# Optimization experiments

Measured on AMD Instinct MI355X. Metric: run time of the kernel, lower is better.

The kernel has to match this reference:

```python
import jax, jax.numpy as jnp
import numpy as np

Q_HEADS, KV_HEADS, DIMS = 16, 4, 1024
HEAD_DIM = DIMS // Q_HEADS          # 64
GROUPS = Q_HEADS // KV_HEADS        # 4


def rope(x):
    # x: [..., s, d]; base-10 thetas, positions start at 1 (per source RoPE)
    s, d = x.shape[-2], x.shape[-1]
    thetas = 10.0 ** (-jnp.arange(d // 2, dtype=jnp.float32))
    angles = jnp.arange(1, s + 1, dtype=jnp.float32)[:, None] * thetas  # [s, d/2]
    cos, sin = jnp.cos(angles), jnp.sin(angles)
    xr, xi = x[..., ::2], x[..., 1::2]
    outr = xr * cos - xi * sin
    outi = xr * sin + xi * cos
    return jnp.stack([outr, outi], axis=-1).reshape(x.shape)  # re-interleave


def setup_inputs() -> dict:
    key = jax.random.key(0)
    ks = jax.random.split(key, 5)
    b, s, in_dim = 4, 2048, 1024
    q = jax.random.normal(ks[0], (b, s, in_dim), dtype=jnp.float32)
    mask = jnp.tril(jnp.ones((s, s), dtype=jnp.float32))  # 1 = keep, 0 = masked
    sc = 1.0 / np.sqrt(in_dim)
    Wq = jax.random.normal(ks[1], (in_dim, Q_HEADS, HEAD_DIM), dtype=jnp.float32) * sc
    Wk = jax.random.normal(ks[2], (in_dim, KV_HEADS, HEAD_DIM), dtype=jnp.float32) * sc
    Wv = jax.random.normal(ks[3], (in_dim, KV_HEADS, HEAD_DIM), dtype=jnp.float32) * sc
    Wo = jax.random.normal(ks[4], (KV_HEADS * HEAD_DIM, in_dim), dtype=jnp.float32) * (1.0 / np.sqrt(KV_HEADS * HEAD_DIM))
    return {"q": q, "mask": mask, "Wq": Wq, "Wk": Wk, "Wv": Wv, "Wo": Wo}


def reference(q, mask, Wq, Wk, Wv, Wo):
    b, s, in_dim = q.shape
    # projections (DenseGeneral, no bias)
    qh = jnp.einsum('bsi,ihd->bshd', q, Wq)   # [b, s, 16, 64]
    kh = jnp.einsum('bsi,ihd->bshd', q, Wk)   # [b, s, 4, 64]  (kv = q)
    vh = jnp.einsum('bsi,ihd->bshd', q, Wv)
    # '... s (h g) d -> ... g h s d' with g=GROUPS
    qh = qh.reshape(b, s, KV_HEADS, GROUPS, HEAD_DIM).transpose(0, 3, 2, 1, 4)  # [b,g,h,s,d]
    kh = kh.transpose(0, 2, 1, 3)  # [b, h, s, d]
    vh = vh.transpose(0, 2, 1, 3)
    qh = rope(qh)
    kh = rope(kh)
    # NOTE: source einsum sums over group axis g
    scores = jnp.einsum('bghsd,bhad->bhsa', qh, kh)  # [b, h, s, s]
    scores = scores - (1.0 / mask - 1.0)             # mask==0 -> -inf
    attn = jax.nn.softmax(scores / jnp.float32(HEAD_DIM ** 0.5), axis=-1)
    out = jnp.einsum('bhsa,bhad->bhsd', attn, vh)    # [b, h, s, d]
    out = out.transpose(0, 2, 1, 3).reshape(b, s, KV_HEADS * HEAD_DIM)
    return out @ Wo  # [b, s, in_dim]
```

## Files before the change

### kernel.cpp

```cpp
#include <hip/hip_runtime.h>
#include <math.h>

#define BATCH 4
#define SEQ   2048
#define DIN   1024
#define KVH   4
#define HD    64
#define MTOT  (BATCH*SEQ)
#define NPROJ 768
#define PROJ_STRIDE (BATCH*KVH*SEQ*HD)
#define NCHUNK_TOT 80

typedef unsigned short ushort_t;
typedef __attribute__((ext_vector_type(8))) short short8;
typedef __attribute__((ext_vector_type(4))) float f32x4;

#define QSCALE (0.125f * 1.44269504088896340736f)

__device__ inline ushort_t f2bf(float x) {
    union { float f; unsigned int u; } v; v.f = x;
    unsigned int r = v.u + 0x7fffu + ((v.u >> 16) & 1u);
    return (ushort_t)(r >> 16);
}
__device__ inline ushort_t f2bf_trunc(float x) {
    return (ushort_t)(__float_as_uint(x) >> 16);
}

__device__ inline void load16_lds(const ushort_t* g, ushort_t* l) {
    __builtin_amdgcn_global_load_lds(
        (const __attribute__((address_space(1))) void*)g,
        (__attribute__((address_space(3))) void*)l, 16, 0, 0);
}

__global__ __launch_bounds__(256) void prep_kernel(
        const float* __restrict__ Wq, const float* __restrict__ Wk,
        const float* __restrict__ Wv, const float* __restrict__ Wo,
        const float* __restrict__ X,
        ushort_t* __restrict__ Wcat_t, ushort_t* __restrict__ Wo_t,
        float2* __restrict__ ctab, ushort_t* __restrict__ Y) {
    const int bx = blockIdx.x;
    const int tid = threadIdx.x;
    if (bx < 4096) {
        int idx = bx * 256 + tid;
        if (idx < NPROJ * DIN) {
            int n = idx >> 10, k = idx & 1023;
            float v;
            if (n < 256) {
                const float* p = Wq + (size_t)k * 1024 + (n >> 6) * 256 + (n & 63);
                v = p[0] + p[64] + p[128] + p[192];
            } else if (n < 512) {
                v = Wk[(size_t)k * 256 + (n - 256)];
            } else {
                v = Wv[(size_t)k * 256 + (n - 512)];
            }
            Wcat_t[idx] = f2bf(v);
        } else {
            int t = idx - NPROJ * DIN;
            int n = t >> 8, k = t & 255;
            Wo_t[t] = f2bf(Wo[(size_t)k * 1024 + n]);
        }
    } else if (bx < 4352) {
        int t = (bx - 4096) * 256 + tid;
        int j = t & 31, s = t >> 5;
        float ang = (float)(s + 1) * exp10f(-(float)j);
        float sn, cs;
        sincosf(ang, &sn, &cs);
        ctab[t] = make_float2(cs, sn);
    } else {
        int i = ((bx - 4352) * 256 + tid) * 4;
        float4 v = *(const float4*)&X[i];
        ushort4 o;
        o.x = f2bf(v.x); o.y = f2bf(v.y); o.z = f2bf(v.z); o.w = f2bf(v.w);
        *(ushort4*)&Y[i] = o;
    }
}

template<int OUT_MODE>
__global__ __launch_bounds__(256) void gemm_mfma_kernel(
        const ushort_t* __restrict__ A, const ushort_t* __restrict__ Bt,
        float* __restrict__ Y, ushort_t* __restrict__ Qbf,
        ushort_t* __restrict__ Kbf, ushort_t* __restrict__ Vt,
        const float2* __restrict__ ctab, int K, int N) {
    __shared__ __align__(16) ushort_t As[128 * 32];
    __shared__ __align__(16) ushort_t Bs[64 * 32];
    const int tid  = threadIdx.x;
    const int w    = tid >> 6, lane = tid & 63;
    const int m15  = lane & 15, quad = lane >> 4;
    const int wm   = (w >> 1) * 64, wn = (w & 1) * 32;
    const int m0   = blockIdx.y * 128, n0 = blockIdx.x * 64;
    const int lr   = lane >> 2;
    const int lc   = (lane & 3) * 8;

    f32x4 acc[4][2];
    #pragma unroll
    for (int i = 0; i < 4; ++i)
        #pragma unroll
        for (int j = 0; j < 2; ++j) acc[i][j] = (f32x4){0.f, 0.f, 0.f, 0.f};

    for (int k0 = 0; k0 < K; k0 += 32) {
        __syncthreads();
        load16_lds(A  + (size_t)(m0 + w * 32 + lr) * K + k0 + lc,      As + w * 1024);
        load16_lds(A  + (size_t)(m0 + w * 32 + 16 + lr) * K + k0 + lc, As + w * 1024 + 512);
        load16_lds(Bt + (size_t)(n0 + w * 16 + lr) * K + k0 + lc,      Bs + w * 512);
        __syncthreads();

        short8 af[4], bfm[2];
        #pragma unroll
        for (int i = 0; i < 4; ++i)
            af[i] = *(const short8*)&As[(wm + i * 16 + m15) * 32 + quad * 8];
        #pragma unroll
        for (int j = 0; j < 2; ++j)
            bfm[j] = *(const short8*)&Bs[(wn + j * 16 + m15) * 32 + quad * 8];
        #pragma unroll
        for (int i = 0; i < 4; ++i)
            #pragma unroll
            for (int j = 0; j < 2; ++j)
                acc[i][j] = __builtin_amdgcn_mfma_f32_16x16x32_bf16(
                                af[i], bfm[j], acc[i][j], 0, 0, 0);
    }

    if (OUT_MODE == 0) {
        #pragma unroll
        for (int i = 0; i < 4; ++i)
            #pragma unroll
            for (int r = 0; r < 4; ++r) {
                size_t row = (size_t)(m0 + wm + i * 16 + quad * 4 + r);
                #pragma unroll
                for (int j = 0; j < 2; ++j)
                    Y[row * N + n0 + wn + j * 16 + m15] = acc[i][j][r];
            }
    } else {
        #pragma unroll
        for (int j = 0; j < 2; ++j) {
            int c = n0 + wn + j * 16 + m15;
            int proj = c >> 8, cc = c & 255;
            int hd = cc >> 6, d = cc & 63;
            if (proj < 2) {
                int jj = d >> 1;
                float sgn = (d & 1) ? 1.0f : -1.0f;
                float qs  = (proj == 0) ? QSCALE : 1.0f;
                ushort_t* dst = (proj ? Kbf : Qbf) + (size_t)hd * SEQ * HD + d;
                #pragma unroll
                for (int i = 0; i < 4; ++i)
                    #pragma unroll
                    for (int r = 0; r < 4; ++r) {
                        int m = m0 + wm + i * 16 + quad * 4 + r;
                        int b = m >> 11, s = m & (SEQ - 1);
                        float x = acc[i][j][r];
                        float p = __shfl_xor(x, 1);
                        float2 ct = ctab[s * 32 + jj];
                        float o = (x * ct.x + sgn * p * ct.y) * qs;
                        dst[(((size_t)b * KVH) * SEQ + s) * HD] = f2bf(o);
                    }
            } else {
                ushort_t* Vp = Vt + (((size_t)hd * HD) + d) * SEQ;
                #pragma unroll
                for (int i = 0; i < 4; ++i)
                    #pragma unroll
                    for (int r = 0; r < 4; ++r) {
                        int m = m0 + wm + i * 16 + quad * 4 + r;
                        int b = m >> 11, s = m & (SEQ - 1);
                        Vp[(size_t)b * KVH * HD * SEQ + s] = f2bf(acc[i][j][r]);
                    }
            }
        }
    }
}

__global__ __launch_bounds__(256) void attn_mfma_kernel(
        const ushort_t* __restrict__ Qbf, const ushort_t* __restrict__ Kbf,
        const ushort_t* __restrict__ Vtbf, float* __restrict__ pO,
        float* __restrict__ pL) {
    __shared__ __align__(16) ushort_t Ks[64][72];
    __shared__ __align__(16) ushort_t Vts[64][72];
    __shared__ __align__(16) ushort_t Ps[4][16][72];
    const int tid  = threadIdx.x;
    const int w    = tid >> 6, lane = tid & 63;
    const int m15  = lane & 15, quad = lane >> 4;
    const int bh   = blockIdx.y;
    const int f    = 79 - blockIdx.x;
    int qt, ch;
    if (f < 8)       { qt = f;                    ch = 0; }
    else if (f < 24) { qt = 8  + ((f - 8) >> 1);  ch = (f - 8) & 1; }
    else if (f < 48) { qt = 16 + (f - 24) / 3;    ch = (f - 24) % 3; }
    else             { qt = 24 + ((f - 48) >> 2); ch = (f - 48) & 3; }
    const int q0 = qt * 64;
    const int kt_beg = ch * 8;
    const int kt_end = min(kt_beg + 8, qt + 1);

    const ushort_t* Qb  = Qbf  + (size_t)bh * SEQ * HD;
    const ushort_t* Kb  = Kbf  + (size_t)bh * SEQ * HD;
    const ushort_t* Vtb = Vtbf + (size_t)bh * HD * SEQ;

    const int qrow = q0 + w * 16 + m15;
    short8 qf0 = *(const short8*)(Qb + (size_t)qrow * HD + quad * 8);
    short8 qf1 = *(const short8*)(Qb + (size_t)qrow * HD + 32 + quad * 8);

    f32x4 o[4];
    #pragma unroll
    for (int nt = 0; nt < 4; ++nt) o[nt] = (f32x4){0.f, 0.f, 0.f, 0.f};
    float lacc[4] = {0.f, 0.f, 0.f, 0.f};

    const int sc_ = tid & 7;
    const int sr_ = tid >> 3;

    short8 pk0, pk1, pv0, pv1;
    {
        const int k0 = kt_beg * 64;
        pk0 = *(const short8*)(Kb  + (size_t)(k0 + sr_) * HD + sc_ * 8);
        pk1 = *(const short8*)(Kb  + (size_t)(k0 + sr_ + 32) * HD + sc_ * 8);
        pv0 = *(const short8*)(Vtb + (size_t)sr_ * SEQ + k0 + sc_ * 8);
        pv1 = *(const short8*)(Vtb + (size_t)(sr_ + 32) * SEQ + k0 + sc_ * 8);
    }

    for (int kt = kt_beg; kt < kt_end; ++kt) {
        const int k0 = kt * 64;
        __syncthreads();
        *(short8*)&Ks[sr_][sc_*8]       = pk0;
        *(short8*)&Ks[sr_ + 32][sc_*8]  = pk1;
        *(short8*)&Vts[sr_][sc_*8]      = pv0;
        *(short8*)&Vts[sr_ + 32][sc_*8] = pv1;
        __syncthreads();

        if (kt + 1 < kt_end) {
            const int kn = k0 + 64;
            pk0 = *(const short8*)(Kb  + (size_t)(kn + sr_) * HD + sc_ * 8);
            pk1 = *(const short8*)(Kb  + (size_t)(kn + sr_ + 32) * HD + sc_ * 8);
            pv0 = *(const short8*)(Vtb + (size_t)sr_ * SEQ + kn + sc_ * 8);
            pv1 = *(const short8*)(Vtb + (size_t)(sr_ + 32) * SEQ + kn + sc_ * 8);
        }

        f32x4 sc4[4];
        #pragma unroll
        for (int nt = 0; nt < 4; ++nt) {
            f32x4 c = {0.f, 0.f, 0.f, 0.f};
            c = __builtin_amdgcn_mfma_f32_16x16x32_bf16(
                    qf0, *(const short8*)&Ks[nt*16 + m15][quad*8], c, 0, 0, 0);
            c = __builtin_amdgcn_mfma_f32_16x16x32_bf16(
                    qf1, *(const short8*)&Ks[nt*16 + m15][32 + quad*8], c, 0, 0, 0);
            sc4[nt] = c;
        }
        if (kt == qt) {
            #pragma unroll
            for (int nt = 0; nt < 4; ++nt) {
                int colg = k0 + nt*16 + m15;
                #pragma unroll
                for (int r = 0; r < 4; ++r) {
                    int rowg = q0 + w*16 + quad*4 + r;
                    if (colg > rowg) sc4[nt][r] = -INFINITY;
                }
            }
        }

        #pragma unroll
        for (int nt = 0; nt < 4; ++nt)
            #pragma unroll
            for (int r = 0; r < 4; ++r) {
                float e = exp2f(sc4[nt][r]);
                lacc[r] += e;
                Ps[w][quad*4 + r][nt*16 + m15] = f2bf_trunc(e);
            }

        short8 pa0 = *(const short8*)&Ps[w][m15][quad*8];
        short8 pa1 = *(const short8*)&Ps[w][m15][32 + quad*8];
        #pragma unroll
        for (int nt = 0; nt < 4; ++nt) {
            o[nt] = __builtin_amdgcn_mfma_f32_16x16x32_bf16(
                        pa0, *(const short8*)&Vts[nt*16 + m15][quad*8], o[nt], 0, 0, 0);
            o[nt] = __builtin_amdgcn_mfma_f32_16x16x32_bf16(
                        pa1, *(const short8*)&Vts[nt*16 + m15][32 + quad*8], o[nt], 0, 0, 0);
        }
    }

    const int blk = bh * NCHUNK_TOT + f;
    #pragma unroll
    for (int r = 0; r < 4; ++r) {
        float ls = lacc[r];
        ls += __shfl_xor(ls, 1);
        ls += __shfl_xor(ls, 2);
        ls += __shfl_xor(ls, 4);
        ls += __shfl_xor(ls, 8);
        int row = w * 16 + quad * 4 + r;
        if (m15 == 0) pL[(size_t)blk * 64 + row] = ls;
        #pragma unroll
        for (int nt = 0; nt < 4; ++nt)
            pO[(size_t)blk * 4096 + row * 64 + nt * 16 + m15] = o[nt][r];
    }
}

__device__ inline int flat_of(int qt, int ch) {
    if (qt < 8)  return qt;
    if (qt < 16) return 8 + (qt - 8) * 2 + ch;
    if (qt < 24) return 24 + (qt - 16) * 3 + ch;
    return 48 + (qt - 24) * 4 + ch;
}

__global__ __launch_bounds__(256) void combine_kernel(
        const float* __restrict__ pO, const float* __restrict__ pL,
        ushort_t* __restrict__ Out) {
    const int qt = blockIdx.x, bh = blockIdx.y;
    const int tid = threadIdx.x;
    const int row = tid >> 2;
    const int cb = (tid & 3) * 16;
    const int nch = (qt >> 3) + 1;
    float acc[16] = {};
    float lsum = 0.f;
    for (int c = 0; c < nch; ++c) {
        int blk = bh * NCHUNK_TOT + flat_of(qt, c);
        const float* po = pO + (size_t)blk * 4096 + row * 64 + cb;
        lsum += pL[(size_t)blk * 64 + row];
        #pragma unroll
        for (int j = 0; j < 4; ++j) {
            float4 v = *(const float4*)&po[j * 4];
            acc[j*4+0] += v.x; acc[j*4+1] += v.y;
            acc[j*4+2] += v.z; acc[j*4+3] += v.w;
        }
    }
    float inv = 1.0f / lsum;
    int b = bh >> 2, h = bh & 3;
    int s = qt * 64 + row;
    ushort_t tmp[16];
    #pragma unroll
    for (int j = 0; j < 16; ++j) tmp[j] = f2bf(acc[j] * inv);
    ushort_t* dst = Out + ((size_t)b * SEQ + s) * (KVH * HD) + h * HD + cb;
    *(uint4*)dst = ((uint4*)tmp)[0];
    *(uint4*)(dst + 8) = ((uint4*)tmp)[1];
}

extern "C" void kernel_launch(void* const* d_in, const int* in_sizes, int n_in,
                              void* d_out, int out_size, void* d_ws, size_t ws_size,
                              hipStream_t stream) {
    const float* q  = (const float*)d_in[0];
    const float* Wq = (const float*)d_in[2];
    const float* Wk = (const float*)d_in[3];
    const float* Wv = (const float*)d_in[4];
    const float* Wo = (const float*)d_in[5];
    float* out = (float*)d_out;

    char* base = (char*)d_ws;
    ushort_t* wcat_t  = (ushort_t*)(base);
    ushort_t* wo_t    = (ushort_t*)(base + 0x180000);
    float2*   ctab    = (float2*)(base + 0x200000);
    ushort_t* qin_bf  = (ushort_t*)(base + 0x280000);
    ushort_t* attn_bf = (ushort_t*)(base + 0x280000);
    float*    pO      = (float*)(base + 0x680000);
    float*    pL      = (float*)(base + 0x1A80000);
    ushort_t* q_bf    = (ushort_t*)(base + 0x1B00000);
    ushort_t* k_bf    = (ushort_t*)(base + 0x1F00000);
    ushort_t* vt_bf   = (ushort_t*)(base + 0x2300000);

    prep_kernel<<<12544, 256, 0, stream>>>(Wq, Wk, Wv, Wo, q,
                                           wcat_t, wo_t, ctab, qin_bf);

    dim3 gproj(NPROJ / 64, MTOT / 128);
    gemm_mfma_kernel<1><<<gproj, 256, 0, stream>>>(
        qin_bf, wcat_t, nullptr, q_bf, k_bf, vt_bf, ctab, DIN, NPROJ);

    dim3 gattn(NCHUNK_TOT, BATCH * KVH);
    attn_mfma_kernel<<<gattn, 256, 0, stream>>>(q_bf, k_bf, vt_bf, pO, pL);

    dim3 gcomb(SEQ / 64, BATCH * KVH);
    combine_kernel<<<gcomb, 256, 0, stream>>>(pO, pL, attn_bf);

    dim3 gout(DIN / 64, MTOT / 128);
    gemm_mfma_kernel<0><<<gout, 256, 0, stream>>>(
        attn_bf, wo_t, out, nullptr, nullptr, nullptr, nullptr, KVH * HD, DIN);
}
```

Baseline: 186.7 us.

## Double GEMM K-tile to 64 with rotated LDS layout to avoid bank conflicts

The GEMM's K step grows from 32 to 64, which halves the number of loop iterations and __syncthreads barriers and gives each staged tile twice as many MFMAs. Shared-memory rows are stored with a per-row rotation of 16-byte chunks, and the fragment read offsets undo that rotation, so that reads across lanes are meant to avoid LDS bank conflicts. In exchange, LDS use per block doubles, which may lower occupancy, and the read swizzle has to match the write pattern exactly to stay correct.

```diff
diff --git a/kernel.cpp b/kernel.cpp
--- a/kernel.cpp
+++ b/kernel.cpp
@@ -81,15 +81,18 @@
         float* __restrict__ Y, ushort_t* __restrict__ Qbf,
         ushort_t* __restrict__ Kbf, ushort_t* __restrict__ Vt,
         const float2* __restrict__ ctab, int K, int N) {
-    __shared__ __align__(16) ushort_t As[128 * 32];
-    __shared__ __align__(16) ushort_t Bs[64 * 32];
+    __shared__ __align__(16) ushort_t As[128 * 64];
+    __shared__ __align__(16) ushort_t Bs[64 * 64];
     const int tid  = threadIdx.x;
     const int w    = tid >> 6, lane = tid & 63;
     const int m15  = lane & 15, quad = lane >> 4;
     const int wm   = (w >> 1) * 64, wn = (w & 1) * 32;
     const int m0   = blockIdx.y * 128, n0 = blockIdx.x * 64;
-    const int lr   = lane >> 2;
-    const int lc   = (lane & 3) * 8;
+    const int r8   = lane >> 3;
+    const int cs   = (((lane & 7) + r8) & 7) * 8;
+    const int rotr = (m15 & 7) * 8;
+    const int off0 = (quad * 8 + 64 - rotr) & 63;
+    const int off1 = (32 + quad * 8 + 64 - rotr) & 63;
 
     f32x4 acc[4][2];
     #pragma unroll
@@ -97,26 +100,38 @@
         #pragma unroll
         for (int j = 0; j < 2; ++j) acc[i][j] = (f32x4){0.f, 0.f, 0.f, 0.f};
 
-    for (int k0 = 0; k0 < K; k0 += 32) {
+    for (int k0 = 0; k0 < K; k0 += 64) {
         __syncthreads();
-        load16_lds(A  + (size_t)(m0 + w * 32 + lr) * K + k0 + lc,      As + w * 1024);
-        load16_lds(A  + (size_t)(m0 + w * 32 + 16 + lr) * K + k0 + lc, As + w * 1024 + 512);
-        load16_lds(Bt + (size_t)(n0 + w * 16 + lr) * K + k0 + lc,      Bs + w * 512);
+        #pragma unroll
+        for (int p = 0; p < 4; ++p)
+            load16_lds(A + (size_t)(m0 + w * 32 + p * 8 + r8) * K + k0 + cs,
+                       As + (w * 32 + p * 8) * 64);
+        #pragma unroll
+        for (int p = 0; p < 2; ++p)
+            load16_lds(Bt + (size_t)(n0 + w * 16 + p * 8 + r8) * K + k0 + cs,
+                       Bs + (w * 16 + p * 8) * 64);
         __syncthreads();
 
-        short8 af[4], bfm[2];
-        #pragma unroll
-        for (int i = 0; i < 4; ++i)
-            af[i] = *(const short8*)&As[(wm + i * 16 + m15) * 32 + quad * 8];
-        #pragma unroll
-        for (int j = 0; j < 2; ++j)
-            bfm[j] = *(const short8*)&Bs[(wn + j * 16 + m15) * 32 + quad * 8];
+        short8 af[4][2], bfm[2][2];
+        #pragma unroll
+        for (int i = 0; i < 4; ++i) {
+            af[i][0] = *(const short8*)&As[(wm + i * 16 + m15) * 64 + off0];
+            af[i][1] = *(const short8*)&As[(wm + i * 16 + m15) * 64 + off1];
+        }
+        #pragma unroll
+        for (int j = 0; j < 2; ++j) {
+            bfm[j][0] = *(const short8*)&Bs[(wn + j * 16 + m15) * 64 + off0];
+            bfm[j][1] = *(const short8*)&Bs[(wn + j * 16 + m15) * 64 + off1];
+        }
         #pragma unroll
         for (int i = 0; i < 4; ++i)
             #pragma unroll
-            for (int j = 0; j < 2; ++j)
+            for (int j = 0; j < 2; ++j) {
                 acc[i][j] = __builtin_amdgcn_mfma_f32_16x16x32_bf16(
-                                af[i], bfm[j], acc[i][j], 0, 0, 0);
+                                af[i][0], bfm[j][0], acc[i][j], 0, 0, 0);
+                acc[i][j] = __builtin_amdgcn_mfma_f32_16x16x32_bf16(
+                                af[i][1], bfm[j][1], acc[i][j], 0, 0, 0);
+            }
     }
 
     if (OUT_MODE == 0) {
```

Result: faster. 178.2 us (-4.5%).
